# Optimization experiments

Measured on AMD Instinct MI355X. Metric: run time of the kernel, lower is better.

Reference implementation:

```python
import jax, jax.numpy as jnp
import numpy as np
from jax import lax

A = 20          # alphabet size (input_size)
L = 512         # max_seq_length
CH = 8          # conv channels
N_LAYERS = 9    # log2(512) conv+pool stages


def setup_inputs() -> dict:
    key = jax.random.key(0)
    ks = jax.random.split(key, 6)
    B = 1024
    idx = jax.random.randint(ks[0], (B, L), 0, A)
    lens = jax.random.randint(ks[1], (B,), L // 4, L + 1)
    masks = jnp.arange(L)[None, :] < lens[:, None]            # [B, L] bool
    # one-hot sequences, zeroed at padded positions (so nonzero() skips them)
    x = jax.nn.one_hot(idx, A, dtype=jnp.float32) * masks[..., None].astype(jnp.float32)
    blosum = jax.random.normal(ks[2], (A, A), jnp.float32)
    blosum = (blosum + blosum.T) * 0.5                        # symmetric like BLOSUM
    lpm = blosum                                              # trainable copy
    pm = jnp.clip(blosum, 0.0)                                # clamp(min=0) constant
    std = jnp.ones((1,), jnp.float32)                         # Gaussian std for row decay
    w0 = jax.random.normal(ks[3], (CH, 1, 3), jnp.float32) * 0.3
    ws = jax.random.normal(ks[4], (N_LAYERS - 1, CH, CH, 3), jnp.float32) * 0.2
    return {"x": x, "masks": masks, "lpm": lpm, "pm": pm, "std": std, "w0": w0, "ws": ws}


def _shift_pos(m, k):
    # target index clamp(s + k, max=L-1): shift right by k, boundary index L-1
    # collects any source in the last k+1 positions (set semantics -> OR).
    head = jnp.zeros(m.shape[:-1] + (k,), dtype=bool)
    body = m[..., : L - k - 1]                                # targets k .. L-2
    last = jnp.any(m[..., L - 1 - k:], axis=-1, keepdims=True)
    return jnp.concatenate([head, body, last], axis=-1)


def _shift_neg(m, k):
    # target index clamp(s - k, min=0)
    first = jnp.any(m[..., : k + 1], axis=-1, keepdims=True)
    body = m[..., k + 1:]                                     # targets 1 .. L-1-k
    tail = jnp.zeros(m.shape[:-1] + (k,), dtype=bool)
    return jnp.concatenate([first, body, tail], axis=-1)


def _column(nz, lpm, pm):
    # Banded substitution scatter: each one-hot row i writes V[i, r] into row r
    # at the same (batch, seq) position. Original nested index_put loops collapse
    # to a single 20x20 matrix V applied via einsum (one-hot => no collisions).
    ii = jnp.arange(A)[:, None]
    rr = jnp.arange(A)[None, :]
    M = jnp.clip(lpm, 0.001, 1.0) * pm
    # up-writes: j in 1..18-i => i < r <= 18 ; down-writes: j in 1..i => r < i
    V = jnp.where((rr > ii) & (rr <= A - 2), M, 0.0) + jnp.where(rr < ii, M.T, 0.0)
    return jnp.einsum('bis,ir->brs', nz, V)


def _row(m, std):
    # Gaussian positional decay: writes exp(-k^2/(2 std^2)) at seq offsets +-k,
    # k = 1,2,3 in order (later k overwrites earlier at clamp collisions).
    row = jnp.zeros(m.shape, jnp.float32)
    for k in (1, 2, 3):
        mk = _shift_pos(m, k) | _shift_neg(m, k)
        vk = jnp.exp(-(k * k) / (2.0 * std * std))[0]
        row = jnp.where(mk, vk, row)
    return row


def _conv1d(h, w):
    # Conv1d(kernel=3, stride=1, pad=1, no bias)
    return lax.conv_general_dilated(h, w, (1,), [(1, 1)],
                                    dimension_numbers=('NCH', 'OIH', 'NCH'))


def _avgpool2(h):
    N, C, Lh = h.shape
    return h.reshape(N, C, Lh // 2, 2).mean(-1)


def reference(x, masks, lpm, pm, std, w0, ws):
    B = x.shape[0]
    xp = jnp.transpose(x, (0, 2, 1))          # [B, 20, L]
    m = xp != 0
    nz = m.astype(xp.dtype)
    h = xp + _column(nz, lpm, pm) + _row(m, std)
    h = h.reshape(B * A, 1, L)
    h = _avgpool2(_conv1d(h, w0))
    for i in range(N_LAYERS - 1):
        h = _avgpool2(_conv1d(h, ws[i]))
    return h.squeeze(-1).reshape(B, A, -1)    # [B, 20, 8]
```

## Files before the change

kernel.cpp:

```cpp
#include <hip/hip_runtime.h>
#include <math.h>

#define LSEQ 512
#define NA 20
#define NCH 8
#define WPAD 516

__global__ void vt_kernel(const float* __restrict__ lpm,
                          const float* __restrict__ pm,
                          float* __restrict__ vtn) {
    int o = threadIdx.x;
    if (o >= NA * NA) return;
    int j = o / NA, a = o % NA;
    float v = 0.f;
    if (a > j && a <= NA - 2)
        v += fminf(fmaxf(lpm[j * NA + a], 0.001f), 1.0f) * pm[j * NA + a];
    if (a < j)
        v += fminf(fmaxf(lpm[a * NA + j], 0.001f), 1.0f) * pm[a * NA + j];
    vtn[o] = v;
}

__global__ __launch_bounds__(64) void wf_kernel(
    const float* __restrict__ w0,
    const float* __restrict__ wsg,
    float* __restrict__ wf)
{
    const int s = blockIdx.x;
    const int t = threadIdx.x;
    if (s >= LSEQ) {
        if (t < NCH) wf[t * WPAD + s] = 0.f;
        return;
    }

    __shared__ float s_h[LSEQ];
    __shared__ float s_a[NCH * 256];
    __shared__ float s_b[NCH * 128];

    for (int i = t; i < LSEQ; i += 64) s_h[i] = (i == s) ? 1.f : 0.f;
    __syncthreads();

    const int c = t >> 3;
    const int pb = t & 7;

    {
        float q0 = w0[c * 3 + 0], q1 = w0[c * 3 + 1], q2 = w0[c * 3 + 2];
        float wa = q0, wb = q0 + q1, wc2 = q1 + q2, wd = q2;
        for (int p = pb; p < 256; p += 8) {
            int xx = 2 * p;
            float x0 = (xx > 0) ? s_h[xx - 1] : 0.f;
            float x1 = s_h[xx];
            float x2 = s_h[xx + 1];
            float x3 = (xx + 2 < LSEQ) ? s_h[xx + 2] : 0.f;
            s_a[c * 256 + p] = 0.5f * (wa * x0 + wb * x1 + wc2 * x2 + wd * x3);
        }
    }
    __syncthreads();

    int Lin = 256;
    for (int li = 0; li < 8; ++li) {
        const float* fin = (li & 1) ? s_b : s_a;
        float* fout = (li & 1) ? s_a : s_b;
        const int Lout = Lin >> 1;

        float wa[8], wb[8], wc2[8], wd[8];
        const float* wl = wsg + li * 192 + c * 24;
#pragma unroll
        for (int ci = 0; ci < 8; ++ci) {
            float q0 = wl[ci * 3 + 0], q1 = wl[ci * 3 + 1], q2 = wl[ci * 3 + 2];
            wa[ci] = q0; wb[ci] = q0 + q1; wc2[ci] = q1 + q2; wd[ci] = q2;
        }

        for (int p = pb; p < Lout; p += 8) {
            int xx = 2 * p;
            float acc = 0.f;
#pragma unroll
            for (int ci = 0; ci < 8; ++ci) {
                const float* ip = fin + ci * Lin + xx;
                float x0 = (xx > 0) ? ip[-1] : 0.f;
                float x1 = ip[0];
                float x2 = ip[1];
                float x3 = (xx + 2 < Lin) ? ip[2] : 0.f;
                acc += wa[ci] * x0 + wb[ci] * x1 + wc2[ci] * x2 + wd[ci] * x3;
            }
            fout[c * Lout + p] = 0.5f * acc;
        }
        __syncthreads();
        Lin = Lout;
    }

    if (t < NCH) wf[t * WPAD + s] = s_a[t];
}

__global__ __launch_bounds__(256) void main_kernel(
    const float* __restrict__ x,
    const float* __restrict__ vtn,
    const float* __restrict__ g_std,
    const float* __restrict__ wf,
    float* __restrict__ out)
{
    const int b = blockIdx.x;
    const int t = threadIdx.x;

    __shared__ __align__(16) float s_h[NA * WPAD];
    __shared__ __align__(16) float s_w[NCH * WPAD];
    __shared__ __align__(16) float s_vtn[NA * NA];
    __shared__ unsigned char s_idx[LSEQ];

    float4* s_x4 = (float4*)s_h;
    const float4* g_x4 = (const float4*)(x + (size_t)b * LSEQ * NA);
#pragma unroll
    for (int i = t; i < LSEQ * NA / 4; i += 256) s_x4[i] = g_x4[i];

    float4* s_w4 = (float4*)s_w;
    const float4* g_w4 = (const float4*)wf;
    for (int i = t; i < NCH * WPAD / 4; i += 256) s_w4[i] = g_w4[i];

    if (t < NA * NA / 4) ((float4*)s_vtn)[t] = ((const float4*)vtn)[t];
    __syncthreads();

    for (int p = t; p < LSEQ; p += 256) {
        int id = 255;
#pragma unroll
        for (int q = 0; q < 5; ++q) {
            float4 v = s_x4[p * 5 + q];
            if (v.x > .5f) id = 4 * q + 0;
            if (v.y > .5f) id = 4 * q + 1;
            if (v.z > .5f) id = 4 * q + 2;
            if (v.w > .5f) id = 4 * q + 3;
        }
        s_idx[p] = (unsigned char)id;
    }
    __syncthreads();

    const float stdv = g_std[0];
    const float inv2s2 = 1.f / (2.f * stdv * stdv);
    const float vks[3] = {__expf(-1.f * inv2s2), __expf(-4.f * inv2s2), __expf(-9.f * inv2s2)};

    for (int s = t; s < LSEQ; s += 256) {
        const int ai = s_idx[s];
        const bool valid = ai < NA;
#pragma unroll
        for (int a = 0; a < NA; ++a) {
            float v = valid ? (s_vtn[ai * NA + a] + (a == ai ? 1.f : 0.f)) : 0.f;
            s_h[a * WPAD + s] = v;
        }
#pragma unroll
        for (int k = 1; k <= 3; ++k) {
            const float add = vks[k - 1];
            if (s == LSEQ - 1) {
                for (int u = LSEQ - 1 - k; u <= LSEQ - 1; ++u) {
                    int tg = s_idx[u];
                    if (tg < NA)
                        s_h[tg * WPAD + s] =
                            (valid ? s_vtn[ai * NA + tg] + (tg == ai ? 1.f : 0.f) : 0.f) + add;
                }
            } else if (s >= k) {
                int tg = s_idx[s - k];
                if (tg < NA)
                    s_h[tg * WPAD + s] =
                        (valid ? s_vtn[ai * NA + tg] + (tg == ai ? 1.f : 0.f) : 0.f) + add;
            }
            if (s == 0) {
                for (int u = 0; u <= k; ++u) {
                    int tg = s_idx[u];
                    if (tg < NA)
                        s_h[tg * WPAD + s] =
                            (valid ? s_vtn[ai * NA + tg] + (tg == ai ? 1.f : 0.f) : 0.f) + add;
                }
            } else if (s + k < LSEQ) {
                int tg = s_idx[s + k];
                if (tg < NA)
                    s_h[tg * WPAD + s] =
                        (valid ? s_vtn[ai * NA + tg] + (tg == ai ? 1.f : 0.f) : 0.f) + add;
            }
        }
    }
    if (t < NA * 4) {
        int a = t >> 2, s = LSEQ + (t & 3);
        s_h[a * WPAD + s] = 0.f;
    }
    __syncthreads();

    if (t < NA * NCH) {
        const int a = t >> 3, c = t & 7;
        const float4* hr = (const float4*)(s_h + a * WPAD);
        const float4* wr = (const float4*)(s_w + c * WPAD);
        float acc = 0.f;
#pragma unroll 3
        for (int j = 0; j < WPAD / 4; ++j) {
            float4 hv = hr[j];
            float4 wv = wr[j];
            acc += hv.x * wv.x + hv.y * wv.y + hv.z * wv.z + hv.w * wv.w;
        }
        out[(size_t)b * (NA * NCH) + t] = acc;
    }
}

extern "C" void kernel_launch(void* const* d_in, const int* in_sizes, int n_in,
                              void* d_out, int out_size, void* d_ws, size_t ws_size,
                              hipStream_t stream) {
    const float* x    = (const float*)d_in[0];
    const float* lpm  = (const float*)d_in[2];
    const float* pm   = (const float*)d_in[3];
    const float* stdp = (const float*)d_in[4];
    const float* w0   = (const float*)d_in[5];
    const float* wsg  = (const float*)d_in[6];
    float* out = (float*)d_out;

    const int B = in_sizes[0] / (LSEQ * NA);

    float* vtn = (float*)d_ws;
    float* wf  = (float*)d_ws + 1024;

    vt_kernel<<<dim3(1), dim3(448), 0, stream>>>(lpm, pm, vtn);
    wf_kernel<<<dim3(WPAD), dim3(64), 0, stream>>>(w0, wsg, wf);
    main_kernel<<<dim3(B), dim3(256), 0, stream>>>(x, vtn, stdp, wf, out);
}
```

Measured before the change: 130.7 us.

## Replace dense feature-map dot product with sparse atomic accumulation over one-hot indices

Drops building the dense 20x512 input map in shared memory in the main kernel. Instead it accumulates, per residue index, the effective-filter weights into small shared arrays with shared-memory atomics, and handles the row-decay terms the same way. The substitution-matrix term is then applied as a 20x20 product on the reduced sums. The x read now goes straight from global memory into index extraction, and the vt and wf precompute kernels are merged into one launch with four impulse responses per block. This removes the large shared-memory fill, the dot-product pass and one launch, but adds atomic contention and duplicate-target logic that has to match the reference overwrite semantics.

```diff
diff --git a/kernel.cpp b/kernel.cpp
--- a/kernel.cpp
+++ b/kernel.cpp
@@ -5,38 +5,41 @@
 #define NA 20
 #define NCH 8
 #define WPAD 516
-
-__global__ void vt_kernel(const float* __restrict__ lpm,
-                          const float* __restrict__ pm,
-                          float* __restrict__ vtn) {
-    int o = threadIdx.x;
-    if (o >= NA * NA) return;
-    int j = o / NA, a = o % NA;
-    float v = 0.f;
-    if (a > j && a <= NA - 2)
-        v += fminf(fmaxf(lpm[j * NA + a], 0.001f), 1.0f) * pm[j * NA + a];
-    if (a < j)
-        v += fminf(fmaxf(lpm[a * NA + j], 0.001f), 1.0f) * pm[a * NA + j];
-    vtn[o] = v;
-}
-
-__global__ __launch_bounds__(64) void wf_kernel(
+#define NBLK_IMP 129
+
+__global__ __launch_bounds__(256) void wf_vt_kernel(
     const float* __restrict__ w0,
     const float* __restrict__ wsg,
-    float* __restrict__ wf)
+    const float* __restrict__ lpm,
+    const float* __restrict__ pm,
+    float* __restrict__ wf,
+    float* __restrict__ vtn)
 {
-    const int s = blockIdx.x;
-    const int t = threadIdx.x;
-    if (s >= LSEQ) {
-        if (t < NCH) wf[t * WPAD + s] = 0.f;
+    if (blockIdx.x == NBLK_IMP) {
+        for (int o = threadIdx.x; o < NA * NA; o += 256) {
+            int j = o / NA, a = o % NA;
+            float v = 0.f;
+            if (a > j && a <= NA - 2)
+                v += fminf(fmaxf(lpm[j * NA + a], 0.001f), 1.0f) * pm[j * NA + a];
+            if (a < j)
+                v += fminf(fmaxf(lpm[a * NA + j], 0.001f), 1.0f) * pm[a * NA + j];
+            vtn[o] = v;
+        }
         return;
     }
 
-    __shared__ float s_h[LSEQ];
-    __shared__ float s_a[NCH * 256];
-    __shared__ float s_b[NCH * 128];
-
-    for (int i = t; i < LSEQ; i += 64) s_h[i] = (i == s) ? 1.f : 0.f;
+    const int w = threadIdx.x >> 6;
+    const int t = threadIdx.x & 63;
+    const int s = blockIdx.x * 4 + w;
+
+    __shared__ float s_h[4][LSEQ];
+    __shared__ float s_a[4][NCH * 256];
+    __shared__ float s_b[4][NCH * 128];
+    float* hh = s_h[w];
+    float* aa = s_a[w];
+    float* bb = s_b[w];
+
+    for (int i = t; i < LSEQ; i += 64) hh[i] = (i == s) ? 1.f : 0.f;
     __syncthreads();
 
     const int c = t >> 3;
@@ -47,19 +50,19 @@
         float wa = q0, wb = q0 + q1, wc2 = q1 + q2, wd = q2;
         for (int p = pb; p < 256; p += 8) {
             int xx = 2 * p;
-            float x0 = (xx > 0) ? s_h[xx - 1] : 0.f;
-            float x1 = s_h[xx];
-            float x2 = s_h[xx + 1];
-            float x3 = (xx + 2 < LSEQ) ? s_h[xx + 2] : 0.f;
-            s_a[c * 256 + p] = 0.5f * (wa * x0 + wb * x1 + wc2 * x2 + wd * x3);
+            float x0 = (xx > 0) ? hh[xx - 1] : 0.f;
+            float x1 = hh[xx];
+            float x2 = hh[xx + 1];
+            float x3 = (xx + 2 < LSEQ) ? hh[xx + 2] : 0.f;
+            aa[c * 256 + p] = 0.5f * (wa * x0 + wb * x1 + wc2 * x2 + wd * x3);
         }
     }
     __syncthreads();
 
     int Lin = 256;
     for (int li = 0; li < 8; ++li) {
-        const float* fin = (li & 1) ? s_b : s_a;
-        float* fout = (li & 1) ? s_a : s_b;
+        const float* fin = (li & 1) ? bb : aa;
+        float* fout = (li & 1) ? aa : bb;
         const int Lout = Lin >> 1;
 
         float wa[8], wb[8], wc2[8], wd[8];
@@ -88,7 +91,7 @@
         Lin = Lout;
     }
 
-    if (t < NCH) wf[t * WPAD + s] = s_a[t];
+    if (t < NCH && s < LSEQ) wf[t * WPAD + s] = aa[t];
 }
 
 __global__ __launch_bounds__(256) void main_kernel(
@@ -100,98 +103,97 @@
 {
     const int b = blockIdx.x;
     const int t = threadIdx.x;
-
-    __shared__ __align__(16) float s_h[NA * WPAD];
+    const int w = t >> 6;
+    const int lane = t & 63;
+    const int c = lane >> 3;
+    const int so = lane & 7;
+
     __shared__ __align__(16) float s_w[NCH * WPAD];
     __shared__ __align__(16) float s_vtn[NA * NA];
+    __shared__ float s_G[4 * NA * NCH];
+    __shared__ float s_R[4 * NA * NCH];
+    __shared__ float s_Gs[NA * NCH];
     __shared__ unsigned char s_idx[LSEQ];
 
-    float4* s_x4 = (float4*)s_h;
-    const float4* g_x4 = (const float4*)(x + (size_t)b * LSEQ * NA);
-#pragma unroll
-    for (int i = t; i < LSEQ * NA / 4; i += 256) s_x4[i] = g_x4[i];
+    for (int e = t; e < 4 * NA * NCH; e += 256) { s_G[e] = 0.f; s_R[e] = 0.f; }
 
     float4* s_w4 = (float4*)s_w;
     const float4* g_w4 = (const float4*)wf;
-    for (int i = t; i < NCH * WPAD / 4; i += 256) s_w4[i] = g_w4[i];
-
+    for (int e = t; e < NCH * WPAD / 4; e += 256) s_w4[e] = g_w4[e];
     if (t < NA * NA / 4) ((float4*)s_vtn)[t] = ((const float4*)vtn)[t];
-    __syncthreads();
-
-    for (int p = t; p < LSEQ; p += 256) {
+
+    const float4* xb = (const float4*)(x + (size_t)b * LSEQ * NA);
+#pragma unroll
+    for (int rep = 0; rep < 2; ++rep) {
+        int s = t + rep * 256;
         int id = 255;
 #pragma unroll
         for (int q = 0; q < 5; ++q) {
-            float4 v = s_x4[p * 5 + q];
+            float4 v = xb[s * 5 + q];
             if (v.x > .5f) id = 4 * q + 0;
             if (v.y > .5f) id = 4 * q + 1;
             if (v.z > .5f) id = 4 * q + 2;
             if (v.w > .5f) id = 4 * q + 3;
         }
-        s_idx[p] = (unsigned char)id;
+        s_idx[s] = (unsigned char)id;
     }
     __syncthreads();
 
     const float stdv = g_std[0];
     const float inv2s2 = 1.f / (2.f * stdv * stdv);
-    const float vks[3] = {__expf(-1.f * inv2s2), __expf(-4.f * inv2s2), __expf(-9.f * inv2s2)};
-
-    for (int s = t; s < LSEQ; s += 256) {
-        const int ai = s_idx[s];
-        const bool valid = ai < NA;
-#pragma unroll
-        for (int a = 0; a < NA; ++a) {
-            float v = valid ? (s_vtn[ai * NA + a] + (a == ai ? 1.f : 0.f)) : 0.f;
-            s_h[a * WPAD + s] = v;
-        }
-#pragma unroll
-        for (int k = 1; k <= 3; ++k) {
-            const float add = vks[k - 1];
-            if (s == LSEQ - 1) {
-                for (int u = LSEQ - 1 - k; u <= LSEQ - 1; ++u) {
-                    int tg = s_idx[u];
-                    if (tg < NA)
-                        s_h[tg * WPAD + s] =
-                            (valid ? s_vtn[ai * NA + tg] + (tg == ai ? 1.f : 0.f) : 0.f) + add;
-                }
-            } else if (s >= k) {
-                int tg = s_idx[s - k];
-                if (tg < NA)
-                    s_h[tg * WPAD + s] =
-                        (valid ? s_vtn[ai * NA + tg] + (tg == ai ? 1.f : 0.f) : 0.f) + add;
-            }
-            if (s == 0) {
-                for (int u = 0; u <= k; ++u) {
-                    int tg = s_idx[u];
-                    if (tg < NA)
-                        s_h[tg * WPAD + s] =
-                            (valid ? s_vtn[ai * NA + tg] + (tg == ai ? 1.f : 0.f) : 0.f) + add;
-                }
-            } else if (s + k < LSEQ) {
-                int tg = s_idx[s + k];
-                if (tg < NA)
-                    s_h[tg * WPAD + s] =
-                        (valid ? s_vtn[ai * NA + tg] + (tg == ai ? 1.f : 0.f) : 0.f) + add;
-            }
-        }
-    }
-    if (t < NA * 4) {
-        int a = t >> 2, s = LSEQ + (t & 3);
-        s_h[a * WPAD + s] = 0.f;
-    }
+    const float v1 = __expf(-1.f * inv2s2);
+    const float v2 = __expf(-4.f * inv2s2);
+    const float v3 = __expf(-9.f * inv2s2);
+
+    float* Gp = s_G + w * (NA * NCH);
+    float* Rp = s_R + w * (NA * NCH);
+#pragma unroll 1
+    for (int it = 0; it < 16; ++it) {
+        const int s = w * 128 + it * 8 + so;
+        const float wv = s_w[c * WPAD + s];
+        const int j = s_idx[s];
+        if (j < NA) atomicAdd(&Gp[j * NCH + c], wv);
+
+        if (s == 0 || s == LSEQ - 1) {
+            const int base = (s == 0) ? 0 : LSEQ - 4;
+            const int u0 = s_idx[base + 0], u1 = s_idx[base + 1];
+            const int u2 = s_idx[base + 2], u3 = s_idx[base + 3];
+            const float a3 = v3 * wv;
+            if (u0 < NA) atomicAdd(&Rp[u0 * NCH + c], a3);
+            if (u1 < NA && u1 != u0) atomicAdd(&Rp[u1 * NCH + c], a3);
+            if (u2 < NA && u2 != u0 && u2 != u1) atomicAdd(&Rp[u2 * NCH + c], a3);
+            if (u3 < NA && u3 != u0 && u3 != u1 && u3 != u2) atomicAdd(&Rp[u3 * NCH + c], a3);
+        } else {
+            const int tp3 = (s >= 3) ? s_idx[s - 3] : 255;
+            const int tn3 = (s + 3 <= LSEQ - 1) ? s_idx[s + 3] : 255;
+            const int tp2 = (s >= 2) ? s_idx[s - 2] : 255;
+            const int tn2 = (s + 2 <= LSEQ - 1) ? s_idx[s + 2] : 255;
+            const int tp1 = s_idx[s - 1];
+            const int tn1 = s_idx[s + 1];
+            if (tp3 < NA) atomicAdd(&Rp[tp3 * NCH + c], v3 * wv);
+            if (tn3 < NA && tn3 != tp3) atomicAdd(&Rp[tn3 * NCH + c], v3 * wv);
+            if (tp2 < NA && tp2 != tp3 && tp2 != tn3)
+                atomicAdd(&Rp[tp2 * NCH + c], v2 * wv);
+            if (tn2 < NA && tn2 != tp3 && tn2 != tn3 && tn2 != tp2)
+                atomicAdd(&Rp[tn2 * NCH + c], v2 * wv);
+            if (tp1 < NA && tp1 != tp3 && tp1 != tn3 && tp1 != tp2 && tp1 != tn2)
+                atomicAdd(&Rp[tp1 * NCH + c], v1 * wv);
+            if (tn1 < NA && tn1 != tp3 && tn1 != tn3 && tn1 != tp2 && tn1 != tn2 && tn1 != tp1)
+                atomicAdd(&Rp[tn1 * NCH + c], v1 * wv);
+        }
+    }
+    __syncthreads();
+
+    if (t < NA * NCH)
+        s_Gs[t] = s_G[t] + s_G[160 + t] + s_G[320 + t] + s_G[480 + t];
     __syncthreads();
 
     if (t < NA * NCH) {
-        const int a = t >> 3, c = t & 7;
-        const float4* hr = (const float4*)(s_h + a * WPAD);
-        const float4* wr = (const float4*)(s_w + c * WPAD);
-        float acc = 0.f;
-#pragma unroll 3
-        for (int j = 0; j < WPAD / 4; ++j) {
-            float4 hv = hr[j];
-            float4 wv = wr[j];
-            acc += hv.x * wv.x + hv.y * wv.y + hv.z * wv.z + hv.w * wv.w;
-        }
+        const int a = t >> 3, cc = t & 7;
+        float acc = s_Gs[t] + s_R[t] + s_R[160 + t] + s_R[320 + t] + s_R[480 + t];
+#pragma unroll
+        for (int j = 0; j < NA; ++j)
+            acc += s_vtn[j * NA + a] * s_Gs[j * NCH + cc];
         out[(size_t)b * (NA * NCH) + t] = acc;
     }
 }
@@ -210,9 +212,8 @@
     const int B = in_sizes[0] / (LSEQ * NA);
 
     float* vtn = (float*)d_ws;
-    float* wf  = (float*)d_ws + 1024;
-
-    vt_kernel<<<dim3(1), dim3(448), 0, stream>>>(lpm, pm, vtn);
-    wf_kernel<<<dim3(WPAD), dim3(64), 0, stream>>>(w0, wsg, wf);
-    main_kernel<<<dim3(B), dim3(256), 0, stream>>>(x, vtn, stdp, wf, out);
+    float* wfb = (float*)d_ws + 1024;
+
+    wf_vt_kernel<<<dim3(NBLK_IMP + 1), dim3(256), 0, stream>>>(w0, wsg, lpm, pm, wfb, vtn);
+    main_kernel<<<dim3(B), dim3(256), 0, stream>>>(x, vtn, stdp, wfb, out);
 }
```

Result: slower. 229.4 us (+75.5%).
